# Performance work log

Hardware: AMD Instinct MI355X
Metric: run time of the kernel (lower is better)

Reference implementation:

```python
import jax, jax.numpy as jnp
import numpy as np

D_MODEL = 512
EPS = 1e-5  # torch LayerNorm default


def _layernorm(x, g, b):
    mu = jnp.mean(x, axis=-1, keepdims=True)
    var = jnp.mean(jnp.square(x - mu), axis=-1, keepdims=True)
    return (x - mu) * jax.lax.rsqrt(var + EPS) * g + b


def setup_inputs() -> dict:
    key = jax.random.key(0)
    ks = jax.random.split(key, 12)
    d = D_MODEL
    s = 1.0 / np.sqrt(d)
    s4 = 1.0 / np.sqrt(4 * d)
    return {
        "x": jax.random.normal(ks[0], (4, 4096, d), dtype=jnp.float32),
        "Wq": jax.random.uniform(ks[1], (d, d), jnp.float32, -s, s),
        "bq": jax.random.uniform(ks[2], (d,), jnp.float32, -s, s),
        "Wk": jax.random.uniform(ks[3], (d, d), jnp.float32, -s, s),
        "bk": jax.random.uniform(ks[4], (d,), jnp.float32, -s, s),
        "Wv": jax.random.uniform(ks[5], (d, d), jnp.float32, -s, s),
        "bv": jax.random.uniform(ks[6], (d,), jnp.float32, -s, s),
        "g1": jnp.ones((d,), jnp.float32),
        "b1": jnp.zeros((d,), jnp.float32),
        "g2": jnp.ones((d,), jnp.float32),
        "b2": jnp.zeros((d,), jnp.float32),
        "W1": jax.random.uniform(ks[7], (d, 4 * d), jnp.float32, -s, s),
        "bf1": jax.random.uniform(ks[8], (4 * d,), jnp.float32, -s, s),
        "W2": jax.random.uniform(ks[9], (4 * d, d), jnp.float32, -s4, s4),
        "bf2": jax.random.uniform(ks[10], (d,), jnp.float32, -s4, s4),
    }


def reference(x, Wq, bq, Wk, bk, Wv, bv, g1, b1, g2, b2, W1, bf1, W2, bf2):
    # QKV projections: [b, s, d]
    Q = jnp.einsum("bsd,de->bse", x, Wq) + bq
    K = jnp.einsum("bsd,de->bse", x, Wk) + bk
    V = jnp.einsum("bsd,de->bse", x, Wv) + bv
    scale = 1.0 / jnp.sqrt(jnp.float32(K.shape[-1]))
    scores = jnp.einsum("bqd,bkd->bqk", Q, K) * scale  # [b, s, s]
    attn = jax.nn.softmax(scores, axis=-1)
    att = jnp.einsum("bqk,bkd->bqd", attn, V)
    x = _layernorm(x + att, g1, b1)
    h = jax.nn.relu(jnp.einsum("bsd,df->bsf", x, W1) + bf1)
    ffn = jnp.einsum("bsf,fd->bsd", h, W2) + bf2
    return _layernorm(x + ffn, g2, b2)
```

## Files before the change

kernel.cpp:

```cpp
#include <hip/hip_runtime.h>
#include <hip/hip_bf16.h>

typedef unsigned short u16;
typedef short bf16x8 __attribute__((ext_vector_type(8)));
typedef float f32x4 __attribute__((ext_vector_type(4)));

__device__ __forceinline__ float b2f(u16 u) {
  union { float f; unsigned int i; } v; v.i = ((unsigned int)u) << 16; return v.f;
}
__device__ __forceinline__ u16 f2b(float f) {
  union { float f; unsigned int i; } v; v.f = f;
  unsigned int r = v.i + 0x7fffu + ((v.i >> 16) & 1u);
  return (u16)(r >> 16);
}
__device__ __forceinline__ u16 to_b(float v) { return f2b(v); }
__device__ __forceinline__ u16 to_b(u16 v) { return v; }
__device__ __forceinline__ float to_f(float v) { return v; }
__device__ __forceinline__ float to_f(u16 v) { return b2f(v); }

__device__ __forceinline__ void gl_lds16(const u16* g, u16* l) {
  __builtin_amdgcn_global_load_lds(
      (const __attribute__((address_space(1))) unsigned int*)g,
      (__attribute__((address_space(3))) unsigned int*)l, 16, 0, 0);
}

template <bool RELU, bool ATOMIC>
__global__ __launch_bounds__(256)
void gemm_nt(const u16* __restrict__ A, const u16* __restrict__ Bt,
             const float* __restrict__ bias, void* __restrict__ Cv,
             int N, int K, int nsplit, int lda, int ldb, int ldc,
             long sA, long sB, long sC, float scale) {
  __shared__ __align__(16) u16 As[128 * 64];
  __shared__ __align__(16) u16 Bs[128 * 64];
  const int z = blockIdx.z;
  const int batch = z / nsplit, split = z - batch * nsplit;
  const int Ks = K / nsplit;
  const u16* Ab = A + (long)batch * sA + (long)split * Ks;
  const u16* Bb = Bt + (long)batch * sB + (long)split * Ks;
  const int m0 = blockIdx.y * 128, n0 = blockIdx.x * 128;
  const int t = threadIdx.x, w = t >> 6, lane = t & 63;
  const int wm = (w >> 1) * 64, wn = (w & 1) * 64;
  const int lr = lane & 15, q = lane >> 4;

  int srow[4], scol[4];
#pragma unroll
  for (int i = 0; i < 4; i++) {
    int n = w * 256 + i * 64 + lane;
    srow[i] = n >> 3;
    scol[i] = (((n & 7) ^ ((n >> 3) & 7)) * 8);
  }

  f32x4 acc[4][4];
#pragma unroll
  for (int i = 0; i < 4; i++)
#pragma unroll
    for (int j = 0; j < 4; j++) acc[i][j] = (f32x4){0.f, 0.f, 0.f, 0.f};

  for (int k0 = 0; k0 < Ks; k0 += 64) {
#pragma unroll
    for (int i = 0; i < 4; i++)
      gl_lds16(Ab + (long)(m0 + srow[i]) * lda + k0 + scol[i], &As[(w * 256 + i * 64) * 8]);
#pragma unroll
    for (int i = 0; i < 4; i++)
      gl_lds16(Bb + (long)(n0 + srow[i]) * ldb + k0 + scol[i], &Bs[(w * 256 + i * 64) * 8]);
    __syncthreads();
#pragma unroll
    for (int kk = 0; kk < 2; kk++) {
      bf16x8 af[4], bfr[4];
#pragma unroll
      for (int i = 0; i < 4; i++) {
        int row = wm + i * 16 + lr;
        af[i] = *(const bf16x8*)&As[row * 64 + (((kk * 4 + q) ^ (row & 7)) * 8)];
      }
#pragma unroll
      for (int j = 0; j < 4; j++) {
        int row = wn + j * 16 + lr;
        bfr[j] = *(const bf16x8*)&Bs[row * 64 + (((kk * 4 + q) ^ (row & 7)) * 8)];
      }
#pragma unroll
      for (int i = 0; i < 4; i++)
#pragma unroll
        for (int j = 0; j < 4; j++)
          acc[i][j] = __builtin_amdgcn_mfma_f32_16x16x32_bf16(af[i], bfr[j], acc[i][j], 0, 0, 0);
    }
    __syncthreads();
  }

#pragma unroll
  for (int j = 0; j < 4; j++) {
    int cg = n0 + wn + j * 16 + lr;
    float bb = (!ATOMIC && bias) ? bias[cg] : 0.0f;
#pragma unroll
    for (int i = 0; i < 4; i++) {
      int rbase = m0 + wm + i * 16 + q * 4;
#pragma unroll
      for (int r = 0; r < 4; r++) {
        float vv = acc[i][j][r] * scale;
        if (ATOMIC) {
          atomicAdd((float*)Cv + (long)batch * sC + (long)(rbase + r) * ldc + cg, vv);
        } else {
          vv += bb;
          if (RELU) vv = fmaxf(vv, 0.0f);
          ((u16*)Cv)[(long)batch * sC + (long)(rbase + r) * ldc + cg] = f2b(vv);
        }
      }
    }
  }
}

#define STAGE_K(kvv, kcc, sel)                                               \
  {                                                                          \
    _Pragma("unroll") for (int rr = 0; rr < 4; rr++)                         \
        gl_lds16(Kbase + (long)((kvv) * 128 + srow[rr]) * 1536 +             \
                     (kcc) * 128 + scol8[rr],                                \
                 &B2[(sel)][ldsd[rr]]);                                      \
  }
#define STAGE_V(kvv, dcc, sel)                                               \
  {                                                                          \
    _Pragma("unroll") for (int rr = 0; rr < 4; rr++)                         \
        gl_lds16(Vtb + (long)((dcc) * 128 + srow[rr]) * 4096 +               \
                     (kvv) * 128 + scol8[rr],                                \
                 &B2[(sel)][ldsd[rr]]);                                      \
  }

__global__ __launch_bounds__(512, 2)
void flash_attn(const u16* __restrict__ QKV, const u16* __restrict__ Vt,
                u16* __restrict__ attp, float* __restrict__ lbp, float scl) {
  __shared__ __align__(16) u16 B2[2][128 * 128];
  __shared__ __align__(16) u16 Pb[128 * 136];
  const int flat = blockIdx.x;
  const int batch = (flat & 7) >> 1, half = flat & 1, qt = flat >> 3;
  const int t = threadIdx.x, w = t >> 6, lane = t & 63;
  const int lr = lane & 15, q = lane >> 4;
  const long rowbase = (long)batch * 4096 + qt * 128;
  const u16* Qrow  = QKV + (rowbase + w * 16 + lr) * 1536;
  const u16* Kbase = QKV + ((long)batch * 4096 + half * 2048) * 1536 + 512;
  const u16* Vtb   = Vt + (long)batch * 512 * 4096 + half * 2048;
  u16* Pw = &Pb[w * (16 * 136)];

  int srow[4], scol8[4], ldsd[4];
#pragma unroll
  for (int rr = 0; rr < 4; rr++) {
    int n = rr * 512 + t;
    srow[rr] = n >> 4;
    scol8[rr] = ((n & 15) ^ ((n >> 4) & 15)) * 8;
    ldsd[rr] = (rr * 512 + w * 64) * 8;
  }

  f32x4 O[32];
#pragma unroll
  for (int i = 0; i < 32; i++) O[i] = (f32x4){0.f, 0.f, 0.f, 0.f};
  float lsum[4] = {0.f, 0.f, 0.f, 0.f};

  STAGE_K(0, 0, 0);
  __syncthreads();
  int par = 0;

  for (int kv = 0; kv < 16; kv++) {
    f32x4 S[8];
#pragma unroll
    for (int j = 0; j < 8; j++) S[j] = (f32x4){0.f, 0.f, 0.f, 0.f};

    for (int kc = 0; kc < 4; kc++) {
      if (kc < 3) { STAGE_K(kv, kc + 1, par ^ 1); }
      else        { STAGE_V(kv, 0, par ^ 1); }
      bf16x8 Qf[4];
#pragma unroll
      for (int ss = 0; ss < 4; ss++)
        Qf[ss] = *(const bf16x8*)(Qrow + kc * 128 + ss * 32 + q * 8);
#pragma unroll
      for (int ss = 0; ss < 4; ss++)
#pragma unroll
        for (int j = 0; j < 8; j++) {
          int row = j * 16 + lr;
          bf16x8 Kf = *(const bf16x8*)&B2[par][row * 128 + (((ss * 4 + q) ^ lr) * 8)];
          S[j] = __builtin_amdgcn_mfma_f32_16x16x32_bf16(Qf[ss], Kf, S[j], 0, 0, 0);
        }
      __syncthreads();
      par ^= 1;
    }

    float psum[4] = {0.f, 0.f, 0.f, 0.f};
#pragma unroll
    for (int j = 0; j < 8; j++)
#pragma unroll
      for (int r = 0; r < 4; r++) {
        float e = __expf(S[j][r] * scl);
        psum[r] += e;
        Pw[(q * 4 + r) * 136 + j * 16 + lr] = f2b(e);
      }
#pragma unroll
    for (int r = 0; r < 4; r++) {
#pragma unroll
      for (int o = 1; o < 16; o <<= 1) psum[r] += __shfl_xor(psum[r], o);
      lsum[r] += psum[r];
    }
    bf16x8 Pf[4];
#pragma unroll
    for (int t4 = 0; t4 < 4; t4++)
      Pf[t4] = *(const bf16x8*)&Pw[lr * 136 + t4 * 32 + q * 8];

    for (int dc = 0; dc < 4; dc++) {
      if (dc < 3)        { STAGE_V(kv, dc + 1, par ^ 1); }
      else if (kv < 15)  { STAGE_K(kv + 1, 0, par ^ 1); }
#pragma unroll
      for (int t4 = 0; t4 < 4; t4++)
#pragma unroll
        for (int j = 0; j < 8; j++) {
          int row = j * 16 + lr;
          bf16x8 Vf = *(const bf16x8*)&B2[par][row * 128 + (((t4 * 4 + q) ^ lr) * 8)];
          O[dc * 8 + j] = __builtin_amdgcn_mfma_f32_16x16x32_bf16(Pf[t4], Vf, O[dc * 8 + j], 0, 0, 0);
        }
      __syncthreads();
      par ^= 1;
    }
  }

  u16* op = attp + (long)half * 16384 * 512;
#pragma unroll
  for (int i = 0; i < 32; i++) {
    int col = (i >> 3) * 128 + (i & 7) * 16 + lr;
#pragma unroll
    for (int r = 0; r < 4; r++)
      op[(rowbase + w * 16 + q * 4 + r) * 512 + col] = f2b(O[i][r]);
  }
  if (lr == 0)
#pragma unroll
    for (int r = 0; r < 4; r++)
      lbp[(long)half * 16384 + rowbase + w * 16 + q * 4 + r] = lsum[r];
}

template <typename TS>
__global__ __launch_bounds__(1024)
void transpose_b(const TS* __restrict__ src, u16* __restrict__ dst,
                 int R, int Cc, int src_ld, long sbs, long dbs) {
  __shared__ u16 tile[32][33];
  int r = blockIdx.y * 32 + threadIdx.y;
  int c = blockIdx.x * 32 + threadIdx.x;
  tile[threadIdx.y][threadIdx.x] = to_b(src[(long)blockIdx.z * sbs + (long)r * src_ld + c]);
  __syncthreads();
  int rr = blockIdx.x * 32 + threadIdx.y;
  int cc = blockIdx.y * 32 + threadIdx.x;
  dst[(long)blockIdx.z * dbs + (long)rr * R + cc] = tile[threadIdx.x][threadIdx.y];
}

__global__ __launch_bounds__(256)
void f32_to_bf16(const float* __restrict__ s, u16* __restrict__ d) {
  long i = ((long)blockIdx.x * 256 + threadIdx.x) * 8;
  float4 a0 = *(const float4*)(s + i);
  float4 a1 = *(const float4*)(s + i + 4);
  u16 tmp[8] = {f2b(a0.x), f2b(a0.y), f2b(a0.z), f2b(a0.w),
                f2b(a1.x), f2b(a1.y), f2b(a1.z), f2b(a1.w)};
  *(uint4*)(d + i) = *(uint4*)tmp;
}

__global__ __launch_bounds__(256)
void add_ln_att(const float* __restrict__ X, const u16* __restrict__ attp,
                const float* __restrict__ lbp,
                const float* __restrict__ g, const float* __restrict__ b,
                u16* __restrict__ O) {
  const int row = blockIdx.x * 4 + (threadIdx.x >> 6);
  const int lane = threadIdx.x & 63;
  const size_t base = (size_t)row * 512 + lane * 8;
  const float inv = 1.0f / (lbp[row] + lbp[16384 + row]);
  uint4 p0 = *(const uint4*)(attp + base);
  uint4 p1 = *(const uint4*)(attp + 16384L * 512 + base);
  const u16* s0 = (const u16*)&p0;
  const u16* s1 = (const u16*)&p1;
  float z[8];
  float s1a = 0.f, s2a = 0.f;
#pragma unroll
  for (int i = 0; i < 8; i++) {
    z[i] = X[base + i] + (b2f(s0[i]) + b2f(s1[i])) * inv;
    s1a += z[i]; s2a += z[i] * z[i];
  }
#pragma unroll
  for (int o = 32; o > 0; o >>= 1) { s1a += __shfl_xor(s1a, o); s2a += __shfl_xor(s2a, o); }
  const float mu = s1a * (1.0f / 512.0f);
  const float var = s2a * (1.0f / 512.0f) - mu * mu;
  const float rstd = rsqrtf(var + 1e-5f);
#pragma unroll
  for (int i = 0; i < 8; i++) {
    int c = lane * 8 + i;
    O[base + i] = f2b((z[i] - mu) * rstd * g[c] + b[c]);
  }
}

__global__ __launch_bounds__(256)
void add_ln_ffn(const u16* __restrict__ X, const u16* __restrict__ P0,
                const u16* __restrict__ P1, const float* __restrict__ eb,
                const float* __restrict__ g, const float* __restrict__ b,
                float* __restrict__ O) {
  const int row = blockIdx.x * 4 + (threadIdx.x >> 6);
  const int lane = threadIdx.x & 63;
  const size_t base = (size_t)row * 512 + lane * 8;
  uint4 xv = *(const uint4*)(X + base);
  uint4 a0 = *(const uint4*)(P0 + base);
  uint4 a1 = *(const uint4*)(P1 + base);
  const u16* xs = (const u16*)&xv;
  const u16* s0 = (const u16*)&a0;
  const u16* s1 = (const u16*)&a1;
  float z[8];
  float s1a = 0.f, s2a = 0.f;
#pragma unroll
  for (int i = 0; i < 8; i++) {
    int c = lane * 8 + i;
    z[i] = b2f(xs[i]) + b2f(s0[i]) + b2f(s1[i]) + eb[c];
    s1a += z[i]; s2a += z[i] * z[i];
  }
#pragma unroll
  for (int o = 32; o > 0; o >>= 1) { s1a += __shfl_xor(s1a, o); s2a += __shfl_xor(s2a, o); }
  const float mu = s1a * (1.0f / 512.0f);
  const float var = s2a * (1.0f / 512.0f) - mu * mu;
  const float rstd = rsqrtf(var + 1e-5f);
#pragma unroll
  for (int i = 0; i < 8; i++) {
    int c = lane * 8 + i;
    O[base + i] = (z[i] - mu) * rstd * g[c] + b[c];
  }
}

__global__ __launch_bounds__(256)
void concat3(const float* __restrict__ a, const float* __restrict__ b,
             const float* __restrict__ c, float* __restrict__ o) {
  int i = threadIdx.x + blockIdx.x * 256;
  if (i < 512) o[i] = a[i];
  else if (i < 1024) o[i] = b[i - 512];
  else if (i < 1536) o[i] = c[i - 1024];
}

extern "C" void kernel_launch(void* const* d_in, const int* in_sizes, int n_in,
                              void* d_out, int out_size, void* d_ws, size_t ws_size,
                              hipStream_t stream) {
  const float* x   = (const float*)d_in[0];
  const float* Wq  = (const float*)d_in[1];
  const float* bq  = (const float*)d_in[2];
  const float* Wk  = (const float*)d_in[3];
  const float* bk  = (const float*)d_in[4];
  const float* Wv  = (const float*)d_in[5];
  const float* bv  = (const float*)d_in[6];
  const float* g1  = (const float*)d_in[7];
  const float* b1  = (const float*)d_in[8];
  const float* g2  = (const float*)d_in[9];
  const float* b2  = (const float*)d_in[10];
  const float* W1  = (const float*)d_in[11];
  const float* bf1 = (const float*)d_in[12];
  const float* W2  = (const float*)d_in[13];
  const float* bf2 = (const float*)d_in[14];
  float* out = (float*)d_out;

  char* ws = (char*)d_ws;
  const size_t MB = 1048576;
  u16*   QKV   = (u16*)(ws + 0);
  u16*   Vt    = (u16*)(ws + 48 * MB);
  u16*   attp  = (u16*)(ws + 64 * MB);
  u16*   h     = (u16*)(ws + 64 * MB);
  float* lbp   = (float*)(ws + 128 * MB);
  u16*   x1    = (u16*)(ws + 129 * MB);
  u16*   ffnp  = (u16*)(ws + 145 * MB);
  u16*   xb    = (u16*)(ws + 145 * MB);
  u16*   wqkvt = (u16*)(ws + 177 * MB);
  u16*   w1t   = wqkvt + 1536 * 512;
  u16*   w2t   = w1t + 2048 * 512;
  float* bqkv  = (float*)(w2t + 512 * 2048);

  dim3 tb(32, 32);
  f32_to_bf16<<<4096, 256, 0, stream>>>(x, xb);
  transpose_b<float><<<dim3(16, 16, 1), tb, 0, stream>>>(Wq, wqkvt,              512, 512, 512, 0, 0);
  transpose_b<float><<<dim3(16, 16, 1), tb, 0, stream>>>(Wk, wqkvt + 512 * 512,  512, 512, 512, 0, 0);
  transpose_b<float><<<dim3(16, 16, 1), tb, 0, stream>>>(Wv, wqkvt + 1024 * 512, 512, 512, 512, 0, 0);
  transpose_b<float><<<dim3(64, 16, 1), tb, 0, stream>>>(W1, w1t, 512, 2048, 2048, 0, 0);
  transpose_b<float><<<dim3(16, 64, 1), tb, 0, stream>>>(W2, w2t, 2048, 512, 512, 0, 0);
  concat3<<<6, 256, 0, stream>>>(bq, bk, bv, bqkv);

  gemm_nt<false, false><<<dim3(12, 128, 1), 256, 0, stream>>>(
      xb, wqkvt, bqkv, QKV, 1536, 512, 1, 512, 512, 1536, 0, 0, 0, 1.0f);

  transpose_b<u16><<<dim3(16, 128, 4), tb, 0, stream>>>(
      QKV + 1024, Vt, 4096, 512, 1536, 4096L * 1536, 512L * 4096);

  const float scl = 0.044194173824159216f;
  flash_attn<<<dim3(256, 1, 1), 512, 0, stream>>>(QKV, Vt, attp, lbp, scl);

  add_ln_att<<<4096, 256, 0, stream>>>(x, attp, lbp, g1, b1, x1);
  gemm_nt<true, false><<<dim3(16, 128, 1), 256, 0, stream>>>(
      x1, w1t, bf1, h, 2048, 512, 1, 512, 512, 2048, 0, 0, 0, 1.0f);
  gemm_nt<false, false><<<dim3(4, 128, 2), 256, 0, stream>>>(
      h, w2t, nullptr, ffnp, 512, 1024, 1, 2048, 2048, 512,
      1024, 1024, 16384L * 512, 1.0f);
  add_ln_ffn<<<4096, 256, 0, stream>>>(
      x1, ffnp, ffnp + 16384L * 512, bf2, g2, b2, out);
}
```

Measured before the change: 584.5 us.

## Replace full syncthreads with partial vmcnt waits and raw barriers in flash attention

Swaps each __syncthreads (which drains every outstanding load) for an explicit s_waitcnt vmcnt(4) followed by s_barrier. This lets the next tile's global-to-LDS prefetch stay in flight while the current tile is consumed. It also unrolls the kc/dc loops and raises wave priority around the MFMA blocks. The risk is correctness: this relies on the vmcnt accounting matching the 4 loads per stage. Dropping the initial sync depends on that same accounting.

Result: faster. 522.1 us (-10.7%).

```diff
diff --git a/kernel.cpp b/kernel.cpp
--- a/kernel.cpp
+++ b/kernel.cpp
@@ -122,6 +122,9 @@
                      (kvv) * 128 + scol8[rr],                                \
                  &B2[(sel)][ldsd[rr]]);                                      \
   }
+#define VMW4()  asm volatile("s_waitcnt vmcnt(4)" ::: "memory")
+#define VMW0()  asm volatile("s_waitcnt vmcnt(0)" ::: "memory")
+#define CFENCE() asm volatile("" ::: "memory")
 
 __global__ __launch_bounds__(512, 2)
 void flash_attn(const u16* __restrict__ QKV, const u16* __restrict__ Vt,
@@ -153,7 +156,6 @@
   float lsum[4] = {0.f, 0.f, 0.f, 0.f};
 
   STAGE_K(0, 0, 0);
-  __syncthreads();
   int par = 0;
 
   for (int kv = 0; kv < 16; kv++) {
@@ -161,9 +163,14 @@
 #pragma unroll
     for (int j = 0; j < 8; j++) S[j] = (f32x4){0.f, 0.f, 0.f, 0.f};
 
+#pragma unroll
     for (int kc = 0; kc < 4; kc++) {
       if (kc < 3) { STAGE_K(kv, kc + 1, par ^ 1); }
       else        { STAGE_V(kv, 0, par ^ 1); }
+      VMW4();
+      __builtin_amdgcn_s_barrier();
+      CFENCE();
+      __builtin_amdgcn_s_setprio(1);
       bf16x8 Qf[4];
 #pragma unroll
       for (int ss = 0; ss < 4; ss++)
@@ -176,7 +183,9 @@
           bf16x8 Kf = *(const bf16x8*)&B2[par][row * 128 + (((ss * 4 + q) ^ lr) * 8)];
           S[j] = __builtin_amdgcn_mfma_f32_16x16x32_bf16(Qf[ss], Kf, S[j], 0, 0, 0);
         }
-      __syncthreads();
+      __builtin_amdgcn_s_setprio(0);
+      CFENCE();
+      __builtin_amdgcn_s_barrier();
       par ^= 1;
     }
 
@@ -200,9 +209,20 @@
     for (int t4 = 0; t4 < 4; t4++)
       Pf[t4] = *(const bf16x8*)&Pw[lr * 136 + t4 * 32 + q * 8];
 
+#pragma unroll
     for (int dc = 0; dc < 4; dc++) {
-      if (dc < 3)        { STAGE_V(kv, dc + 1, par ^ 1); }
-      else if (kv < 15)  { STAGE_K(kv + 1, 0, par ^ 1); }
+      if (dc < 3) {
+        STAGE_V(kv, dc + 1, par ^ 1);
+        VMW4();
+      } else if (kv < 15) {
+        STAGE_K(kv + 1, 0, par ^ 1);
+        VMW4();
+      } else {
+        VMW0();
+      }
+      __builtin_amdgcn_s_barrier();
+      CFENCE();
+      __builtin_amdgcn_s_setprio(1);
 #pragma unroll
       for (int t4 = 0; t4 < 4; t4++)
 #pragma unroll
@@ -211,7 +231,9 @@
           bf16x8 Vf = *(const bf16x8*)&B2[par][row * 128 + (((t4 * 4 + q) ^ lr) * 8)];
           O[dc * 8 + j] = __builtin_amdgcn_mfma_f32_16x16x32_bf16(Pf[t4], Vf, O[dc * 8 + j], 0, 0, 0);
         }
-      __syncthreads();
+      __builtin_amdgcn_s_setprio(0);
+      CFENCE();
+      __builtin_amdgcn_s_barrier();
       par ^= 1;
     }
   }
```
